# Optimization experiments

Measured on AMD Instinct MI355X. Metric: run time of the kernel, lower is better.

The kernel has to match this reference:

```python
import jax, jax.numpy as jnp
import numpy as np

TEMPERATURE = 1.0
EXAGGERATION = 1.0


def setup_inputs() -> dict:
    key = jax.random.key(0)
    features = jax.random.normal(key, (8192, 128), dtype=jnp.float32)
    return {"features": features}


def _cauchy_sim(x, y):
    # 1 / ((cdist(x,y) * t)^2 + 1) == 1 / (t^2 * sq_dist + 1)
    sq = (
        jnp.sum(x * x, axis=1)[:, None]
        + jnp.sum(y * y, axis=1)[None, :]
        - 2.0 * (x @ y.T)
    )
    sq = jnp.maximum(sq, 0.0)  # numerical floor, matches cdist >= 0
    return 1.0 / (sq * (TEMPERATURE * TEMPERATURE) + 1.0)


def reference(features):
    batch_size = features.shape[0] // 2
    a = features[:batch_size]
    b = features[batch_size:]

    sim_aa = _cauchy_sim(a, a)  # [B, B]
    sim_bb = _cauchy_sim(b, b)  # [B, B]
    sim_ab = _cauchy_sim(a, b)  # [B, B]

    tempered_alignment = jnp.mean(jnp.log(jnp.diagonal(sim_ab)))

    self_mask = jnp.eye(batch_size, dtype=bool)
    sim_aa = jnp.where(self_mask, 0.0, sim_aa)
    sim_bb = jnp.where(self_mask, 0.0, sim_bb)

    # hstack((sim_ab.T, sim_bb)).sum(1) == sim_ab.sum(0) + sim_bb.sum(1)
    logsumexp_1 = jnp.mean(jnp.log(jnp.sum(sim_ab, axis=0) + jnp.sum(sim_bb, axis=1)))
    logsumexp_2 = jnp.mean(jnp.log(jnp.sum(sim_aa, axis=1) + jnp.sum(sim_ab, axis=1)))
    raw_uniformity = logsumexp_1 + logsumexp_2

    loss = -(EXAGGERATION * tempered_alignment - raw_uniformity / 2.0)
    return loss
```

## Files before the change

### kernel.cpp

```cpp
#include <hip/hip_runtime.h>
#include <hip/hip_bf16.h>

typedef __bf16 bf16x8 __attribute__((ext_vector_type(8)));
typedef float  f32x4  __attribute__((ext_vector_type(4)));

static constexpr int D     = 128;
static constexpr int BATCH = 4096;
static constexpr int N     = 8192;
static constexpr int BT    = 128;
static constexpr int NT    = N / BT;
static constexpr int TRI   = NT * (NT + 1) / 2;

__device__ __forceinline__ void load_lds16(const void* g, void* l) {
    __builtin_amdgcn_global_load_lds(
        (const __attribute__((address_space(1))) unsigned int*)g,
        (__attribute__((address_space(3))) unsigned int*)l, 16, 0, 0);
}

__global__ __launch_bounds__(256) void prep_kernel(const float* __restrict__ f,
                                                   unsigned short* __restrict__ fb,
                                                   float* __restrict__ norms,
                                                   float* __restrict__ diag,
                                                   float* __restrict__ out) {
    if (blockIdx.x == 0 && threadIdx.x == 0) out[0] = 0.f;
    const int w = threadIdx.x >> 6, lane = threadIdx.x & 63;
    const int i = blockIdx.x * 4 + w;
    const float2 va = *(const float2*)(f + (size_t)i * D + lane * 2);
    const float2 vb = *(const float2*)(f + (size_t)(i + BATCH) * D + lane * 2);
    union { __bf16 h[2]; unsigned int u; } pa, pb;
    pa.h[0] = (__bf16)va.x; pa.h[1] = (__bf16)va.y;
    pb.h[0] = (__bf16)vb.x; pb.h[1] = (__bf16)vb.y;
    *(unsigned int*)(fb + (size_t)i * D + lane * 2) = pa.u;
    *(unsigned int*)(fb + (size_t)(i + BATCH) * D + lane * 2) = pb.u;
    float na = va.x * va.x + va.y * va.y;
    float nb = vb.x * vb.x + vb.y * vb.y;
    const float dx = va.x - vb.x, dy = va.y - vb.y;
    float dd = dx * dx + dy * dy;
    #pragma unroll
    for (int m = 1; m <= 32; m <<= 1) {
        na += __shfl_xor(na, m); nb += __shfl_xor(nb, m); dd += __shfl_xor(dd, m);
    }
    if (lane == 0) {
        norms[i] = na; norms[i + BATCH] = nb;
        diag[i] = 1.f / (dd + 1.f);
    }
}

__global__ __launch_bounds__(256, 4) void tile_kernel(const unsigned short* __restrict__ fbf,
                                                      const float* __restrict__ norms,
                                                      float* __restrict__ P) {
    const int id = blockIdx.x;
    int ti = (int)((sqrtf(8.f * (float)id + 1.f) - 1.f) * 0.5f);
    while ((ti + 1) * (ti + 2) / 2 <= id) ++ti;
    while (ti * (ti + 1) / 2 > id) --ti;
    const int tj = id - ti * (ti + 1) / 2;
    const bool diagblk = (ti == tj);

    __shared__ __align__(16) unsigned char As[BT * 128];
    __shared__ __align__(16) unsigned char Bs[BT * 128];
    __shared__ float colbuf[BT];

    const int tid = threadIdx.x, wv = tid >> 6, lane = tid & 63;
    const int lr = lane & 15, hk = lane >> 4;

    if (tid < BT) colbuf[tid] = 0.f;

    const unsigned char* Ab = (const unsigned char*)fbf + (size_t)ti * BT * 256;
    const unsigned char* Bb = (const unsigned char*)fbf + (size_t)tj * BT * 256;

    f32x4 acc[2][8];
    #pragma unroll
    for (int i = 0; i < 2; ++i)
        #pragma unroll
        for (int j = 0; j < 8; ++j)
            acc[i][j] = (f32x4){0.f, 0.f, 0.f, 0.f};

    #pragma unroll
    for (int kp = 0; kp < 2; ++kp) {
        if (kp) __syncthreads();
        #pragma unroll
        for (int it = 0; it < 4; ++it) {
            const int cid = it * 256 + tid;
            const int row = cid >> 3, p = cid & 7;
            const int src = row * 256 + kp * 128 + ((p ^ (row & 7)) << 4);
            load_lds16(Ab + src, As + it * 4096 + wv * 1024);
        }
        #pragma unroll
        for (int it = 0; it < 4; ++it) {
            const int cid = it * 256 + tid;
            const int row = cid >> 3, p = cid & 7;
            const int src = row * 256 + kp * 128 + ((p ^ (row & 7)) << 4);
            load_lds16(Bb + src, Bs + it * 4096 + wv * 1024);
        }
        __syncthreads();

        #pragma unroll
        for (int ks = 0; ks < 2; ++ks) {
            const int c = ks * 4 + hk;
            bf16x8 av[2], bv[8];
            #pragma unroll
            for (int fi = 0; fi < 2; ++fi) {
                const int row = wv * 32 + fi * 16 + lr;
                av[fi] = *(const bf16x8*)(As + row * 128 + ((c ^ (row & 7)) << 4));
            }
            #pragma unroll
            for (int fj = 0; fj < 8; ++fj) {
                const int row = fj * 16 + lr;
                bv[fj] = *(const bf16x8*)(Bs + row * 128 + ((c ^ (row & 7)) << 4));
            }
            #pragma unroll
            for (int fi = 0; fi < 2; ++fi)
                #pragma unroll
                for (int fj = 0; fj < 8; ++fj)
                    acc[fi][fj] = __builtin_amdgcn_mfma_f32_16x16x32_bf16(av[fi], bv[fj], acc[fi][fj], 0, 0, 0);
        }
    }

    float colN[8];
    #pragma unroll
    for (int fj = 0; fj < 8; ++fj)
        colN[fj] = norms[tj * BT + fj * 16 + lr];

    float* PR = P + ((size_t)ti * NT + tj) * BT;
    #pragma unroll
    for (int fi = 0; fi < 2; ++fi) {
        const int lrow = wv * 32 + fi * 16 + hk * 4;
        const f32x4 rN = *(const f32x4*)(norms + ti * BT + lrow);
        f32x4 rs = (f32x4){0.f, 0.f, 0.f, 0.f};
        #pragma unroll
        for (int fj = 0; fj < 8; ++fj) {
            const int lcol = fj * 16 + lr;
            #pragma unroll
            for (int r = 0; r < 4; ++r) {
                float sq = rN[r] + colN[fj] - 2.f * acc[fi][fj][r];
                sq = fmaxf(sq, 0.f);
                float sim = __builtin_amdgcn_rcpf(sq + 1.f);
                if (diagblk && (lrow + r == lcol)) sim = 0.f;
                rs[r] += sim;
                acc[fi][fj][r] = sim;
            }
        }
        #pragma unroll
        for (int r = 0; r < 4; ++r) {
            rs[r] += __shfl_xor(rs[r], 1);
            rs[r] += __shfl_xor(rs[r], 2);
            rs[r] += __shfl_xor(rs[r], 4);
            rs[r] += __shfl_xor(rs[r], 8);
        }
        if (lr == 0)
            *(f32x4*)(PR + lrow) = rs;
    }

    if (!diagblk) {
        #pragma unroll
        for (int fj = 0; fj < 8; ++fj) {
            float cs = 0.f;
            #pragma unroll
            for (int fi = 0; fi < 2; ++fi)
                #pragma unroll
                for (int r = 0; r < 4; ++r)
                    cs += acc[fi][fj][r];
            cs += __shfl_xor(cs, 16);
            cs += __shfl_xor(cs, 32);
            if (hk == 0)
                atomicAdd(&colbuf[fj * 16 + lr], cs);
        }
        __syncthreads();
        if (tid < BT)
            P[((size_t)tj * NT + ti) * BT + tid] = colbuf[tid];
    }
}

__global__ __launch_bounds__(128) void finalize_kernel(const float* __restrict__ P,
                                                       const float* __restrict__ diag,
                                                       float* __restrict__ out) {
    const int t = blockIdx.x;
    const int r = threadIdx.x;
    const float* base = P + (size_t)t * NT * BT + r;
    float s = 0.f;
    #pragma unroll 8
    for (int k = 0; k < NT; ++k) s += base[k * BT];
    const int i = t * BT + r;
    float term = 0.5f * __logf(s);
    if (i >= BATCH) term -= __logf(diag[i - BATCH]);
    #pragma unroll
    for (int m = 1; m <= 32; m <<= 1) term += __shfl_xor(term, m);
    if ((threadIdx.x & 63) == 0)
        atomicAdd(out, term / (float)BATCH);
}

extern "C" void kernel_launch(void* const* d_in, const int* in_sizes, int n_in,
                              void* d_out, int out_size, void* d_ws, size_t ws_size,
                              hipStream_t stream) {
    const float* feat = (const float*)d_in[0];
    char* ws = (char*)d_ws;
    unsigned short* fbf = (unsigned short*)ws;
    float* norms = (float*)(ws + (2u << 20));
    float* diag  = (float*)(ws + (2u << 20) + 32768);
    float* P     = (float*)(ws + (2u << 20) + 49152);
    float* out   = (float*)d_out;

    prep_kernel<<<BATCH / 4, 256, 0, stream>>>(feat, fbf, norms, diag, out);
    tile_kernel<<<TRI, 256, 0, stream>>>(fbf, norms, P);
    finalize_kernel<<<NT, 128, 0, stream>>>(P, diag, out);
}
```

Before: 84.77 us.

## Prepack operands into MFMA-ready layouts and double-buffer B tile loads

The prep kernel now writes two pre-swizzled bf16 copies of the features: one laid out so each wave loads its A fragments straight from global memory into registers, and one laid out in 8KB K-phase chunks for LDS staging. The tile kernel drops the A tile from LDS, double-buffers B across four K phases with explicit vmcnt waits and barriers so global loads overlap the MFMA work, and remaps block ids to spread tiles across XCDs. This aims to cut LDS traffic and load-latency stalls, at the cost of twice the workspace, more prep stores, and hand-tuned waitcnt logic that could be fragile.

Result: no change. 85.61 us (+1.0%).

```diff
diff --git a/kernel.cpp b/kernel.cpp
--- a/kernel.cpp
+++ b/kernel.cpp
@@ -17,8 +17,16 @@
         (__attribute__((address_space(3))) unsigned int*)l, 16, 0, 0);
 }
 
+#define WAITV(n) do { asm volatile("s_waitcnt vmcnt(" #n ")" ::: "memory"); \
+                      __builtin_amdgcn_sched_barrier(0); } while (0)
+#define BAR()    do { __builtin_amdgcn_s_barrier(); \
+                      __builtin_amdgcn_sched_barrier(0); } while (0)
+#define LGKM0()  do { asm volatile("s_waitcnt lgkmcnt(0)" ::: "memory"); \
+                      __builtin_amdgcn_sched_barrier(0); } while (0)
+
 __global__ __launch_bounds__(256) void prep_kernel(const float* __restrict__ f,
-                                                   unsigned short* __restrict__ fb,
+                                                   unsigned short* __restrict__ Apack,
+                                                   unsigned short* __restrict__ Bpack,
                                                    float* __restrict__ norms,
                                                    float* __restrict__ diag,
                                                    float* __restrict__ out) {
@@ -30,8 +38,21 @@
     union { __bf16 h[2]; unsigned int u; } pa, pb;
     pa.h[0] = (__bf16)va.x; pa.h[1] = (__bf16)va.y;
     pb.h[0] = (__bf16)vb.x; pb.h[1] = (__bf16)vb.y;
-    *(unsigned int*)(fb + (size_t)i * D + lane * 2) = pa.u;
-    *(unsigned int*)(fb + (size_t)(i + BATCH) * D + lane * 2) = pb.u;
+
+    const int g   = lane >> 2;
+    const int off = (lane & 3) * 4;
+    auto store2 = [&](int row, unsigned int bits) {
+        char* ap = (char*)Apack + ((size_t)(row >> 4)) * 4096 + g * 256 + (row & 15) * 16 + off;
+        *(unsigned int*)ap = bits;
+        const int pair = (row >> 1) & 63, k = row & 1;
+        const int ph = g >> 2, c = g & 3;
+        const int u = ((k << 2) | c) ^ (pair & 7);
+        char* bp = (char*)Bpack + (size_t)(row >> 7) * 32768 + ph * 8192 + (pair * 8 + u) * 16 + off;
+        *(unsigned int*)bp = bits;
+    };
+    store2(i, pa.u);
+    store2(i + BATCH, pb.u);
+
     float na = va.x * va.x + va.y * va.y;
     float nb = vb.x * vb.x + vb.y * vb.y;
     const float dx = va.x - vb.x, dy = va.y - vb.y;
@@ -46,27 +67,27 @@
     }
 }
 
-__global__ __launch_bounds__(256, 4) void tile_kernel(const unsigned short* __restrict__ fbf,
+__global__ __launch_bounds__(256, 4) void tile_kernel(const unsigned short* __restrict__ Apack,
+                                                      const unsigned short* __restrict__ Bpack,
                                                       const float* __restrict__ norms,
                                                       float* __restrict__ P) {
-    const int id = blockIdx.x;
+    const int bid = blockIdx.x;
+    const int id = (bid & 7) * (TRI / 8) + (bid >> 3);
     int ti = (int)((sqrtf(8.f * (float)id + 1.f) - 1.f) * 0.5f);
     while ((ti + 1) * (ti + 2) / 2 <= id) ++ti;
     while (ti * (ti + 1) / 2 > id) --ti;
     const int tj = id - ti * (ti + 1) / 2;
     const bool diagblk = (ti == tj);
 
-    __shared__ __align__(16) unsigned char As[BT * 128];
-    __shared__ __align__(16) unsigned char Bs[BT * 128];
+    __shared__ __align__(16) unsigned char Bs[2][8192];
     __shared__ float colbuf[BT];
 
     const int tid = threadIdx.x, wv = tid >> 6, lane = tid & 63;
     const int lr = lane & 15, hk = lane >> 4;
-
     if (tid < BT) colbuf[tid] = 0.f;
 
-    const unsigned char* Ab = (const unsigned char*)fbf + (size_t)ti * BT * 256;
-    const unsigned char* Bb = (const unsigned char*)fbf + (size_t)tj * BT * 256;
+    const char* Bb = (const char*)Bpack + (size_t)tj * 32768;
+    const char* Ab = (const char*)Apack + (size_t)(ti * 8 + wv * 2) * 4096;
 
     f32x4 acc[2][8];
     #pragma unroll
@@ -75,45 +96,61 @@
         for (int j = 0; j < 8; ++j)
             acc[i][j] = (f32x4){0.f, 0.f, 0.f, 0.f};
 
-    #pragma unroll
-    for (int kp = 0; kp < 2; ++kp) {
-        if (kp) __syncthreads();
-        #pragma unroll
-        for (int it = 0; it < 4; ++it) {
-            const int cid = it * 256 + tid;
-            const int row = cid >> 3, p = cid & 7;
-            const int src = row * 256 + kp * 128 + ((p ^ (row & 7)) << 4);
-            load_lds16(Ab + src, As + it * 4096 + wv * 1024);
-        }
-        #pragma unroll
-        for (int it = 0; it < 4; ++it) {
-            const int cid = it * 256 + tid;
-            const int row = cid >> 3, p = cid & 7;
-            const int src = row * 256 + kp * 128 + ((p ^ (row & 7)) << 4);
-            load_lds16(Bb + src, Bs + it * 4096 + wv * 1024);
-        }
-        __syncthreads();
-
-        #pragma unroll
-        for (int ks = 0; ks < 2; ++ks) {
-            const int c = ks * 4 + hk;
-            bf16x8 av[2], bv[8];
-            #pragma unroll
-            for (int fi = 0; fi < 2; ++fi) {
-                const int row = wv * 32 + fi * 16 + lr;
-                av[fi] = *(const bf16x8*)(As + row * 128 + ((c ^ (row & 7)) << 4));
-            }
-            #pragma unroll
-            for (int fj = 0; fj < 8; ++fj) {
-                const int row = fj * 16 + lr;
-                bv[fj] = *(const bf16x8*)(Bs + row * 128 + ((c ^ (row & 7)) << 4));
-            }
-            #pragma unroll
-            for (int fi = 0; fi < 2; ++fi)
-                #pragma unroll
-                for (int fj = 0; fj < 8; ++fj)
-                    acc[fi][fj] = __builtin_amdgcn_mfma_f32_16x16x32_bf16(av[fi], bv[fj], acc[fi][fj], 0, 0, 0);
-        }
+    #define STAGE(PH) do { \
+        load_lds16(Bb + (PH) * 8192 + tid * 16,        &Bs[(PH) & 1][(tid >> 6) * 1024]); \
+        load_lds16(Bb + (PH) * 8192 + 4096 + tid * 16, &Bs[(PH) & 1][4096 + (tid >> 6) * 1024]); \
+    } while (0)
+
+    #define AV_LOAD(AV, I) do { \
+        AV[0] = *(const bf16x8*)(Ab +        ((I) * 4 + hk) * 256 + lr * 16); \
+        AV[1] = *(const bf16x8*)(Ab + 4096 + ((I) * 4 + hk) * 256 + lr * 16); \
+    } while (0)
+
+    #define BV_READ(BV, PH) do { \
+        const int u_ = (((lr & 1) << 2) | hk) ^ ((lr >> 1) & 7); \
+        const int b_ = (lr >> 1) * 128 + u_ * 16; \
+        _Pragma("unroll") \
+        for (int fj = 0; fj < 8; ++fj) \
+            BV[fj] = *(const bf16x8*)&Bs[(PH) & 1][fj * 1024 + b_]; \
+    } while (0)
+
+    #define MFMA_PH(AV, BV) do { \
+        _Pragma("unroll") \
+        for (int fj = 0; fj < 8; ++fj) { \
+            acc[0][fj] = __builtin_amdgcn_mfma_f32_16x16x32_bf16(AV[0], BV[fj], acc[0][fj], 0, 0, 0); \
+            acc[1][fj] = __builtin_amdgcn_mfma_f32_16x16x32_bf16(AV[1], BV[fj], acc[1][fj], 0, 0, 0); \
+        } \
+    } while (0)
+
+    bf16x8 av0[2], av1[2], av2[2], av3[2];
+
+    STAGE(0); AV_LOAD(av0, 0);
+    STAGE(1); AV_LOAD(av1, 1);
+    WAITV(4); BAR();
+
+    { bf16x8 bv[8];
+      BV_READ(bv, 0); LGKM0(); BAR();
+      STAGE(2); AV_LOAD(av2, 2);
+      MFMA_PH(av0, bv);
+    }
+    WAITV(4); BAR();
+
+    { bf16x8 bv[8];
+      BV_READ(bv, 1); LGKM0(); BAR();
+      STAGE(3); AV_LOAD(av3, 3);
+      MFMA_PH(av1, bv);
+    }
+    WAITV(4); BAR();
+
+    { bf16x8 bv[8];
+      BV_READ(bv, 2); LGKM0(); BAR();
+      MFMA_PH(av2, bv);
+    }
+    WAITV(0); BAR();
+
+    { bf16x8 bv[8];
+      BV_READ(bv, 3); LGKM0();
+      MFMA_PH(av3, bv);
     }
 
     float colN[8];
@@ -169,6 +206,10 @@
         if (tid < BT)
             P[((size_t)tj * NT + ti) * BT + tid] = colbuf[tid];
     }
+    #undef STAGE
+    #undef AV_LOAD
+    #undef BV_READ
+    #undef MFMA_PH
 }
 
 __global__ __launch_bounds__(128) void finalize_kernel(const float* __restrict__ P,
@@ -194,13 +235,14 @@
                               hipStream_t stream) {
     const float* feat = (const float*)d_in[0];
     char* ws = (char*)d_ws;
-    unsigned short* fbf = (unsigned short*)ws;
-    float* norms = (float*)(ws + (2u << 20));
-    float* diag  = (float*)(ws + (2u << 20) + 32768);
-    float* P     = (float*)(ws + (2u << 20) + 49152);
+    unsigned short* Apack = (unsigned short*)ws;
+    unsigned short* Bpack = (unsigned short*)(ws + (2u << 20));
+    float* norms = (float*)(ws + (4u << 20));
+    float* diag  = (float*)(ws + (4u << 20) + 32768);
+    float* P     = (float*)(ws + (4u << 20) + 49152);
     float* out   = (float*)d_out;
 
-    prep_kernel<<<BATCH / 4, 256, 0, stream>>>(feat, fbf, norms, diag, out);
-    tile_kernel<<<TRI, 256, 0, stream>>>(fbf, norms, P);
+    prep_kernel<<<BATCH / 4, 256, 0, stream>>>(feat, Apack, Bpack, norms, diag, out);
+    tile_kernel<<<TRI, 256, 0, stream>>>(Apack, Bpack, norms, P);
     finalize_kernel<<<NT, 128, 0, stream>>>(P, diag, out);
 }
```

## Pre-pack bf16 features into MFMA fragment layout and read operands directly from global

Applied to the files above, without the earlier changes.

The prep kernel now writes bf16 features in a tiled layout that matches the MFMA operand fragment order. The tile kernel then drops its LDS staging and barriers and loads A/B fragments straight from global memory with coalesced 16-byte loads, relying on L2/L1 for reuse. The block index is also remapped with a stride of 8, presumably to spread adjacent tiles across XCDs for better cache locality. The cost is more global and cache traffic per block, since B tiles are re-read by all four waves instead of being shared through LDS.

After: 95.46 us. 12.6% more time.

```diff
diff --git a/kernel.cpp b/kernel.cpp
--- a/kernel.cpp
+++ b/kernel.cpp
@@ -11,14 +11,8 @@
 static constexpr int NT    = N / BT;
 static constexpr int TRI   = NT * (NT + 1) / 2;
 
-__device__ __forceinline__ void load_lds16(const void* g, void* l) {
-    __builtin_amdgcn_global_load_lds(
-        (const __attribute__((address_space(1))) unsigned int*)g,
-        (__attribute__((address_space(3))) unsigned int*)l, 16, 0, 0);
-}
-
 __global__ __launch_bounds__(256) void prep_kernel(const float* __restrict__ f,
-                                                   unsigned short* __restrict__ fb,
+                                                   unsigned short* __restrict__ Fpack,
                                                    float* __restrict__ norms,
                                                    float* __restrict__ diag,
                                                    float* __restrict__ out) {
@@ -30,8 +24,17 @@
     union { __bf16 h[2]; unsigned int u; } pa, pb;
     pa.h[0] = (__bf16)va.x; pa.h[1] = (__bf16)va.y;
     pb.h[0] = (__bf16)vb.x; pb.h[1] = (__bf16)vb.y;
-    *(unsigned int*)(fb + (size_t)i * D + lane * 2) = pa.u;
-    *(unsigned int*)(fb + (size_t)(i + BATCH) * D + lane * 2) = pb.u;
+
+    const int c   = lane >> 2;
+    const int off = (lane & 3) * 4;
+    auto storeF = [&](int row, unsigned int bits) {
+        char* p = (char*)Fpack + (size_t)(row >> 7) * 32768 + ((row >> 5) & 3) * 8192
+                + (c >> 2) * 2048 + ((row >> 4) & 1) * 1024 + (c & 3) * 256 + (row & 15) * 16 + off;
+        *(unsigned int*)p = bits;
+    };
+    storeF(i, pa.u);
+    storeF(i + BATCH, pb.u);
+
     float na = va.x * va.x + va.y * va.y;
     float nb = vb.x * vb.x + vb.y * vb.y;
     const float dx = va.x - vb.x, dy = va.y - vb.y;
@@ -46,27 +49,27 @@
     }
 }
 
-__global__ __launch_bounds__(256, 4) void tile_kernel(const unsigned short* __restrict__ fbf,
+__global__ __launch_bounds__(256, 4) void tile_kernel(const unsigned short* __restrict__ Fpack,
                                                       const float* __restrict__ norms,
                                                       float* __restrict__ P) {
-    const int id = blockIdx.x;
+    const int bid = blockIdx.x;
+    const int id = (bid & 7) * (TRI / 8) + (bid >> 3);
     int ti = (int)((sqrtf(8.f * (float)id + 1.f) - 1.f) * 0.5f);
     while ((ti + 1) * (ti + 2) / 2 <= id) ++ti;
     while (ti * (ti + 1) / 2 > id) --ti;
     const int tj = id - ti * (ti + 1) / 2;
     const bool diagblk = (ti == tj);
 
-    __shared__ __align__(16) unsigned char As[BT * 128];
-    __shared__ __align__(16) unsigned char Bs[BT * 128];
     __shared__ float colbuf[BT];
 
     const int tid = threadIdx.x, wv = tid >> 6, lane = tid & 63;
     const int lr = lane & 15, hk = lane >> 4;
+    if (tid < BT) colbuf[tid] = 0.f;
+    __syncthreads();
 
-    if (tid < BT) colbuf[tid] = 0.f;
-
-    const unsigned char* Ab = (const unsigned char*)fbf + (size_t)ti * BT * 256;
-    const unsigned char* Bb = (const unsigned char*)fbf + (size_t)tj * BT * 256;
+    const char* Ab = (const char*)Fpack + (size_t)ti * 32768 + wv * 8192;
+    const char* Bb = (const char*)Fpack + (size_t)tj * 32768;
+    const int lo = hk * 256 + lr * 16;
 
     f32x4 acc[2][8];
     #pragma unroll
@@ -76,43 +79,17 @@
             acc[i][j] = (f32x4){0.f, 0.f, 0.f, 0.f};
 
     #pragma unroll
-    for (int kp = 0; kp < 2; ++kp) {
-        if (kp) __syncthreads();
+    for (int ks = 0; ks < 4; ++ks) {
+        bf16x8 av[2], bv[8];
+        av[0] = *(const bf16x8*)(Ab + ks * 2048 + lo);
+        av[1] = *(const bf16x8*)(Ab + ks * 2048 + 1024 + lo);
         #pragma unroll
-        for (int it = 0; it < 4; ++it) {
-            const int cid = it * 256 + tid;
-            const int row = cid >> 3, p = cid & 7;
-            const int src = row * 256 + kp * 128 + ((p ^ (row & 7)) << 4);
-            load_lds16(Ab + src, As + it * 4096 + wv * 1024);
-        }
+        for (int fj = 0; fj < 8; ++fj)
+            bv[fj] = *(const bf16x8*)(Bb + (fj >> 1) * 8192 + ks * 2048 + (fj & 1) * 1024 + lo);
         #pragma unroll
-        for (int it = 0; it < 4; ++it) {
-            const int cid = it * 256 + tid;
-            const int row = cid >> 3, p = cid & 7;
-            const int src = row * 256 + kp * 128 + ((p ^ (row & 7)) << 4);
-            load_lds16(Bb + src, Bs + it * 4096 + wv * 1024);
-        }
-        __syncthreads();
-
-        #pragma unroll
-        for (int ks = 0; ks < 2; ++ks) {
-            const int c = ks * 4 + hk;
-            bf16x8 av[2], bv[8];
-            #pragma unroll
-            for (int fi = 0; fi < 2; ++fi) {
-                const int row = wv * 32 + fi * 16 + lr;
-                av[fi] = *(const bf16x8*)(As + row * 128 + ((c ^ (row & 7)) << 4));
-            }
-            #pragma unroll
-            for (int fj = 0; fj < 8; ++fj) {
-                const int row = fj * 16 + lr;
-                bv[fj] = *(const bf16x8*)(Bs + row * 128 + ((c ^ (row & 7)) << 4));
-            }
-            #pragma unroll
-            for (int fi = 0; fi < 2; ++fi)
-                #pragma unroll
-                for (int fj = 0; fj < 8; ++fj)
-                    acc[fi][fj] = __builtin_amdgcn_mfma_f32_16x16x32_bf16(av[fi], bv[fj], acc[fi][fj], 0, 0, 0);
+        for (int fj = 0; fj < 8; ++fj) {
+            acc[0][fj] = __builtin_amdgcn_mfma_f32_16x16x32_bf16(av[0], bv[fj], acc[0][fj], 0, 0, 0);
+            acc[1][fj] = __builtin_amdgcn_mfma_f32_16x16x32_bf16(av[1], bv[fj], acc[1][fj], 0, 0, 0);
         }
     }
 
@@ -194,13 +171,13 @@
                               hipStream_t stream) {
     const float* feat = (const float*)d_in[0];
     char* ws = (char*)d_ws;
-    unsigned short* fbf = (unsigned short*)ws;
+    unsigned short* Fpack = (unsigned short*)ws;
     float* norms = (float*)(ws + (2u << 20));
     float* diag  = (float*)(ws + (2u << 20) + 32768);
     float* P     = (float*)(ws + (2u << 20) + 49152);
     float* out   = (float*)d_out;
 
-    prep_kernel<<<BATCH / 4, 256, 0, stream>>>(feat, fbf, norms, diag, out);
-    tile_kernel<<<TRI, 256, 0, stream>>>(fbf, norms, P);
+    prep_kernel<<<BATCH / 4, 256, 0, stream>>>(feat, Fpack, norms, diag, out);
+    tile_kernel<<<TRI, 256, 0, stream>>>(Fpack, norms, P);
     finalize_kernel<<<NT, 128, 0, stream>>>(P, diag, out);
 }
```
